# Optimization experiments

Hardware: AMD Instinct MI355X
Metric: run time of the kernel (lower is better)

The kernel has to match this reference:

```python
import jax, jax.numpy as jnp
import numpy as np

D_MODEL, D_K, D_V, H = 1024, 64, 64, 16
B, NQ, NK = 2, 2048, 2048


def setup_inputs() -> dict:
    key = jax.random.key(0)
    ks = jax.random.split(key, 12)
    hd = H * D_K
    xav = lambda k, shape: jax.random.uniform(k, shape, jnp.float32, -1.0, 1.0) * np.sqrt(6.0 / (shape[0] + shape[1]))
    return {
        "queries": jax.random.normal(ks[0], (B, NQ, D_MODEL), jnp.float32),
        "keys": jax.random.normal(ks[1], (B, NK, D_MODEL), jnp.float32),
        "values": jax.random.normal(ks[2], (B, NK, D_MODEL), jnp.float32),
        "memory": jax.random.uniform(ks[3], (B, NK), jnp.float32),
        "Wq": xav(ks[4], (D_MODEL, hd)), "bq": jnp.zeros((hd,), jnp.float32),
        "Wk": xav(ks[5], (D_MODEL, hd)), "bk": jnp.zeros((hd,), jnp.float32),
        "Wv": xav(ks[6], (D_MODEL, H * D_V)), "bv": jnp.zeros((H * D_V,), jnp.float32),
        "Wo": xav(ks[7], (H * D_V, D_MODEL)), "bo": jnp.zeros((D_MODEL,), jnp.float32),
        "Wmm": xav(ks[8], (1, H * D_V)), "bmm": jnp.zeros((H * D_V,), jnp.float32),
    }


def reference(queries, keys, values, memory, Wq, bq, Wk, bk, Wv, bv, Wo, bo, Wmm, bmm):
    b, nq = queries.shape[:2]
    nk = keys.shape[1]
    # projections -> (b, h, n, d)
    q = (queries @ Wq + bq).reshape(b, nq, H, D_K).transpose(0, 2, 1, 3)
    k = (keys @ Wk + bk).reshape(b, nk, H, D_K).transpose(0, 2, 1, 3)
    v = (values @ Wv + bv).reshape(b, nk, H, D_V).transpose(0, 2, 1, 3)
    # memory gate: fc_mm(memory[..., None]) -> (b, nk, h*d_k) -> (b, h, nk, d_k)
    mm = (memory[:, :, None] * Wmm[0] + bmm).reshape(b, nk, H, D_K).transpose(0, 2, 1, 3)
    att = jnp.einsum("bhqd,bhkd->bhqk", q, k * mm) / np.sqrt(D_K).astype(np.float32)
    att = jax.nn.softmax(att, axis=-1)
    out = jnp.einsum("bhqk,bhkd->bhqd", att, v * mm)
    out = out.transpose(0, 2, 1, 3).reshape(b, nq, H * D_V)
    return out @ Wo + bo
```

## Files before the change

### kernel.cpp

```cpp
#include <hip/hip_runtime.h>
#include <hip/hip_bf16.h>

#define H_   16
#define NQ_  2048
#define NK_  2048
#define DM_  1024

typedef float f32x4 __attribute__((ext_vector_type(4)));
typedef float f32x16 __attribute__((ext_vector_type(16)));
typedef __bf16 bf16x8 __attribute__((ext_vector_type(8)));
typedef unsigned short u16x8 __attribute__((ext_vector_type(8)));
typedef unsigned short u16x4 __attribute__((ext_vector_type(4)));

__device__ __forceinline__ unsigned short bfbits(float x) {
  __bf16 h = (__bf16)x;
  return __builtin_bit_cast(unsigned short, h);
}

__global__ __launch_bounds__(256) void prep(
    const float* __restrict__ Wq, const float* __restrict__ Wk,
    const float* __restrict__ Wv, const float* __restrict__ Wo,
    unsigned short* __restrict__ WqT, unsigned short* __restrict__ WkT,
    unsigned short* __restrict__ WvT, unsigned short* __restrict__ WoT,
    const float* __restrict__ q, const float* __restrict__ k, const float* __restrict__ v,
    unsigned short* __restrict__ qo, unsigned short* __restrict__ ko,
    unsigned short* __restrict__ vo) {
  __shared__ float t[64][65];
  const int flat = blockIdx.x;
  if (flat < 1024) {
    const int z = flat >> 8, bx = (flat >> 4) & 15, by = flat & 15;
    const float* src = (z == 0) ? Wq : (z == 1) ? Wk : (z == 2) ? Wv : Wo;
    unsigned short* dst = (z == 0) ? WqT : (z == 1) ? WkT : (z == 2) ? WvT : WoT;
    const int r0 = bx * 64, c0 = by * 64;
    for (int i = threadIdx.x; i < 4096; i += 256) {
      int r = i >> 6, c = i & 63;
      t[r][c] = src[(size_t)(r0 + r) * DM_ + c0 + c];
    }
    __syncthreads();
    for (int i = threadIdx.x; i < 4096; i += 256) {
      int n = i >> 6, kk = i & 63;
      dst[(size_t)(c0 + n) * DM_ + r0 + kk] = bfbits(t[kk][n]);
    }
  } else {
    const int tt = flat - 1024;
    const int which = tt >> 11;
    const float* src = (which == 0) ? q : (which == 1) ? k : v;
    unsigned short* dst = (which == 0) ? qo : (which == 1) ? ko : vo;
    const int i = (tt & 2047) * 256 + threadIdx.x;
    const float4* s4 = (const float4*)src;
    float4 a = s4[2 * i], b = s4[2 * i + 1];
    bf16x8 o;
    o[0] = (__bf16)a.x; o[1] = (__bf16)a.y; o[2] = (__bf16)a.z; o[3] = (__bf16)a.w;
    o[4] = (__bf16)b.x; o[5] = (__bf16)b.y; o[6] = (__bf16)b.z; o[7] = (__bf16)b.w;
    *((bf16x8*)dst + i) = o;
  }
}

__device__ __forceinline__ void gll16(const unsigned short* g, unsigned short* l) {
  __builtin_amdgcn_global_load_lds((const __attribute__((address_space(1))) void*)g,
                                   (__attribute__((address_space(3))) void*)l, 16, 0, 0);
}

template <int MODE>
__device__ __forceinline__ void gemm128_body(
    int bx, int by,
    const unsigned short* __restrict__ A, const unsigned short* __restrict__ Bt, int K,
    const float* __restrict__ bias, const float* __restrict__ mem,
    const float* __restrict__ Wmm, const float* __restrict__ bmm,
    unsigned short* __restrict__ obf,
    unsigned short* Al, unsigned short* Bl) {
  const int tid = threadIdx.x, lane = tid & 63, w = tid >> 6;
  const int wm = w >> 1, wn = w & 1;
  const int m0 = bx * 128, n0 = by * 128;
  const int lrow = lane >> 2, lcol = (lane & 3) * 8;
  const int fr = lane & 15, fk = (lane >> 4) * 8;
  constexpr int TSZ = 128 * 32;

  f32x4 acc[4][4] = {};

  const unsigned short* ag0 = A + (size_t)(m0 + w * 32 + lrow) * K + lcol;
  const unsigned short* bg0 = Bt + (size_t)(n0 + w * 32 + lrow) * K + lcol;
  const int oa0 = (w * 32) * 32, oa1 = (w * 32 + 16) * 32;
  const size_t s16K = (size_t)16 * K;

  const int KT = K >> 5;
  gll16(ag0, Al + oa0); gll16(ag0 + s16K, Al + oa1);
  gll16(bg0, Bl + oa0); gll16(bg0 + s16K, Bl + oa1);
  ag0 += 32; bg0 += 32;
  __syncthreads();

  for (int kt = 0; kt < KT; ++kt) {
    const int cb = (kt & 1) * TSZ;
    const int sb = TSZ - cb;
    if (kt + 1 < KT) {
      gll16(ag0, Al + sb + oa0); gll16(ag0 + s16K, Al + sb + oa1);
      gll16(bg0, Bl + sb + oa0); gll16(bg0 + s16K, Bl + sb + oa1);
      ag0 += 32; bg0 += 32;
    }
    bf16x8 af[4], bfr[4];
#pragma unroll
    for (int i = 0; i < 4; ++i)
      af[i] = *(const bf16x8*)&Al[cb + (wm * 64 + i * 16 + fr) * 32 + fk];
#pragma unroll
    for (int j = 0; j < 4; ++j)
      bfr[j] = *(const bf16x8*)&Bl[cb + (wn * 64 + j * 16 + fr) * 32 + fk];
#pragma unroll
    for (int i = 0; i < 4; ++i)
#pragma unroll
      for (int j = 0; j < 4; ++j)
        acc[i][j] = __builtin_amdgcn_mfma_f32_16x16x32_bf16(af[i], bfr[j], acc[i][j], 0, 0, 0);
    __syncthreads();
  }

#pragma unroll
  for (int i = 0; i < 4; ++i) {
    const int rowb = m0 + wm * 64 + i * 16 + (lane >> 4) * 4;
#pragma unroll
    for (int j = 0; j < 4; ++j) {
      const int col = n0 + wn * 64 + j * 16 + fr;
#pragma unroll
      for (int r = 0; r < 4; ++r) {
        float v = acc[i][j][r];
        int rr = rowb + r;
        if (MODE == 0) {
          int b = rr >> 11, nq = rr & 2047, h = col >> 6, d = col & 63;
          float val = (v + bias[col]) * 0.180336884f;
          obf[(((size_t)(b * H_ + h)) * NQ_ + nq) * 64 + d] = bfbits(val);
        } else if (MODE == 1) {
          int b = rr >> 11, nk = rr & 2047, h = col >> 6, d = col & 63;
          float gate = mem[b * NK_ + nk] * Wmm[col] + bmm[col];
          float val = (v + bias[col]) * gate;
          obf[(((size_t)(b * H_ + h)) * NK_ + nk) * 64 + d] = bfbits(val);
        } else {
          int b = col >> 11, key = col & 2047, h = rr >> 6, d = rr & 63;
          float gate = mem[b * NK_ + key] * Wmm[rr] + bmm[rr];
          float val = (v + bias[rr]) * gate;
          int keyp = (key & ~12) | ((key & 4) << 1) | ((key & 8) >> 1);
          obf[(((size_t)(b * H_ + h)) * 64 + d) * NK_ + keyp] = bfbits(val);
        }
      }
    }
  }
}

__global__ __launch_bounds__(256) void gemm_qkv3(
    const unsigned short* __restrict__ qbf, const unsigned short* __restrict__ kbf,
    const unsigned short* __restrict__ vbf, const unsigned short* __restrict__ WvT,
    const unsigned short* __restrict__ WqT, const unsigned short* __restrict__ WkT,
    const float* __restrict__ bq, const float* __restrict__ bk, const float* __restrict__ bv,
    const float* __restrict__ mem, const float* __restrict__ Wmm, const float* __restrict__ bmm,
    unsigned short* __restrict__ Qp, unsigned short* __restrict__ Kp,
    unsigned short* __restrict__ VpT) {
  __shared__ unsigned short Al[2 * 128 * 32];
  __shared__ unsigned short Bl[2 * 128 * 32];
  const int gid = (blockIdx.x & 7) * 96 + (blockIdx.x >> 3);
  if (gid < 256) {
    gemm128_body<0>(gid & 31, gid >> 5, qbf, WqT, 1024, bq, nullptr, nullptr, nullptr,
                    Qp, Al, Bl);
  } else if (gid < 512) {
    int bb = gid - 256;
    gemm128_body<1>(bb & 31, bb >> 5, kbf, WkT, 1024, bk, mem, Wmm, bmm, Kp, Al, Bl);
  } else {
    int bb = gid - 512;
    gemm128_body<2>(bb & 7, bb >> 3, WvT, vbf, 1024, bv, mem, Wmm, bmm, VpT, Al, Bl);
  }
}

__global__ __launch_bounds__(256) void gemm_out(
    const unsigned short* __restrict__ AO, const unsigned short* __restrict__ WoT,
    const float* __restrict__ bo, float* __restrict__ out) {
  __shared__ unsigned short Al[2 * 64 * 32];
  __shared__ unsigned short Bl[2 * 128 * 32];
  const int b = (blockIdx.x & 7) * 64 + (blockIdx.x >> 3);
  const int bx = b & 63, by = b >> 6;
  const int tid = threadIdx.x, lane = tid & 63, w = tid >> 6;
  const int wm = w >> 1, wn = w & 1;
  const int m0 = bx * 64, n0 = by * 128;
  const int lrow = lane >> 2, lcol = (lane & 3) * 8;
  const int fr = lane & 15, fk = (lane >> 4) * 8;
  const int K = 1024;
  constexpr int TA = 64 * 32, TB = 128 * 32;

  f32x4 acc[2][4] = {};

  const unsigned short* ag = AO + (size_t)(m0 + w * 16 + lrow) * K + lcol;
  const unsigned short* bg = WoT + (size_t)(n0 + w * 32 + lrow) * K + lcol;
  const int oa = (w * 16) * 32;
  const int ob0 = (w * 32) * 32, ob1 = (w * 32 + 16) * 32;
  const size_t s16K = (size_t)16 * K;

  gll16(ag, Al + oa);
  gll16(bg, Bl + ob0); gll16(bg + s16K, Bl + ob1);
  ag += 32; bg += 32;
  __syncthreads();

  for (int kt = 0; kt < 32; ++kt) {
    const int ca = (kt & 1) * TA, cbb = (kt & 1) * TB;
    const int sa = TA - ca, sbb = TB - cbb;
    if (kt + 1 < 32) {
      gll16(ag, Al + sa + oa);
      gll16(bg, Bl + sbb + ob0); gll16(bg + s16K, Bl + sbb + ob1);
      ag += 32; bg += 32;
    }
    bf16x8 af[2], bfr[4];
#pragma unroll
    for (int i = 0; i < 2; ++i)
      af[i] = *(const bf16x8*)&Al[ca + (wm * 32 + i * 16 + fr) * 32 + fk];
#pragma unroll
    for (int j = 0; j < 4; ++j)
      bfr[j] = *(const bf16x8*)&Bl[cbb + (wn * 64 + j * 16 + fr) * 32 + fk];
#pragma unroll
    for (int i = 0; i < 2; ++i)
#pragma unroll
      for (int j = 0; j < 4; ++j)
        acc[i][j] = __builtin_amdgcn_mfma_f32_16x16x32_bf16(af[i], bfr[j], acc[i][j], 0, 0, 0);
    __syncthreads();
  }

#pragma unroll
  for (int i = 0; i < 2; ++i) {
    const int rowb = m0 + wm * 32 + i * 16 + (lane >> 4) * 4;
#pragma unroll
    for (int j = 0; j < 4; ++j) {
      const int col = n0 + wn * 64 + j * 16 + fr;
#pragma unroll
      for (int r = 0; r < 4; ++r)
        out[(size_t)(rowb + r) * DM_ + col] = acc[i][j][r] + bo[col];
    }
  }
}

__global__ __launch_bounds__(256, 2) void flash_attn(const unsigned short* __restrict__ Qp,
                                                     const unsigned short* __restrict__ Kp,
                                                     const unsigned short* __restrict__ VpT,
                                                     unsigned short* __restrict__ AO) {
  __shared__ unsigned short Ks[2][128][66];
  __shared__ unsigned short Vs[2][64][130];

  const int tid = threadIdx.x, lane = tid & 63, w = tid >> 6;
  const int gid = (blockIdx.x & 7) * 64 + (blockIdx.x >> 3);
  const int bh = gid >> 4;
  const int qt = gid & 15;
  const int r31 = lane & 31, hi2 = lane >> 5;

  const unsigned short* qg = Qp + (((size_t)bh * NQ_) + qt * 128 + w * 32 + r31) * 64 + hi2 * 8;
  bf16x8 qf[4];
#pragma unroll
  for (int s = 0; s < 4; ++s) qf[s] = *(const bf16x8*)&qg[s * 16];

  const int krow = tid >> 1, kcol = (tid & 1) * 32;
  const int vrow = tid >> 2, vcol = (tid & 3) * 32;
  const unsigned short* kg = Kp + ((size_t)bh * NK_ + krow) * 64 + kcol;
  const unsigned short* vg = VpT + ((size_t)bh * 64 + vrow) * NK_ + vcol;

  f32x16 acc0 = {}, acc1 = {};
  float l_run = 0.0f;

  u16x8 kr[4], vr[4];
#pragma unroll
  for (int i = 0; i < 4; ++i) {
    kr[i] = *(const u16x8*)(kg + 8 * i);
    vr[i] = *(const u16x8*)(vg + 8 * i);
  }
#pragma unroll
  for (int i = 0; i < 4; ++i) {
    *(u16x8*)&Ks[0][krow][kcol + 8 * i] = kr[i];
    *(u16x8*)&Vs[0][vrow][vcol + 8 * i] = vr[i];
  }

  for (int kt = 0; kt < 16; ++kt) {
    const int cur = kt & 1;
    __syncthreads();

    f32x16 sv[4] = {};
    __builtin_amdgcn_s_setprio(1);
#pragma unroll
    for (int s = 0; s < 4; ++s) {
#pragma unroll
      for (int kb = 0; kb < 4; ++kb) {
        bf16x8 ka = *(const bf16x8*)&Ks[cur][kb * 32 + r31][s * 16 + hi2 * 8];
        sv[kb] = __builtin_amdgcn_mfma_f32_32x32x16_bf16(ka, qf[s], sv[kb], 0, 0, 0);
      }
    }
    __builtin_amdgcn_s_setprio(0);

    if (kt + 1 < 16) {
      const unsigned short* kn = kg + (size_t)(kt + 1) * 128 * 64;
      const unsigned short* vn = vg + (kt + 1) * 128;
#pragma unroll
      for (int i = 0; i < 4; ++i) {
        kr[i] = *(const u16x8*)(kn + 8 * i);
        vr[i] = *(const u16x8*)(vn + 8 * i);
      }
    }

    float psp[4] = {0.f, 0.f, 0.f, 0.f};
    bf16x8 pb[8];
#pragma unroll
    for (int kb = 0; kb < 4; ++kb) {
#pragma unroll
      for (int g = 0; g < 16; ++g) {
        float p = __builtin_amdgcn_exp2f(sv[kb][g]);
        psp[kb] += p;
        pb[2 * kb + (g >> 3)][g & 7] = (__bf16)p;
      }
    }
    float ps = (psp[0] + psp[1]) + (psp[2] + psp[3]);
    ps += __shfl_xor(ps, 32);
    l_run += ps;

    __builtin_amdgcn_s_setprio(1);
#pragma unroll
    for (int ks = 0; ks < 8; ++ks) {
      bf16x8 va0 = *(const bf16x8*)&Vs[cur][r31][ks * 16 + hi2 * 8];
      bf16x8 va1 = *(const bf16x8*)&Vs[cur][32 + r31][ks * 16 + hi2 * 8];
      acc0 = __builtin_amdgcn_mfma_f32_32x32x16_bf16(va0, pb[ks], acc0, 0, 0, 0);
      acc1 = __builtin_amdgcn_mfma_f32_32x32x16_bf16(va1, pb[ks], acc1, 0, 0, 0);
    }
    __builtin_amdgcn_s_setprio(0);

    if (kt + 1 < 16) {
#pragma unroll
      for (int i = 0; i < 4; ++i) {
        *(u16x8*)&Ks[cur ^ 1][krow][kcol + 8 * i] = kr[i];
        *(u16x8*)&Vs[cur ^ 1][vrow][vcol + 8 * i] = vr[i];
      }
    }
  }

  const int b = bh >> 4, h = bh & 15;
  const float linv = 1.0f / l_run;
  const int qrow = qt * 128 + w * 32 + r31;
  const size_t rowbase = (((size_t)b * NQ_ + qrow) << 10) + h * 64;
#pragma unroll
  for (int c = 0; c < 4; ++c) {
    u16x4 o0, o1;
#pragma unroll
    for (int i = 0; i < 4; ++i) {
      o0[i] = bfbits(acc0[c * 4 + i] * linv);
      o1[i] = bfbits(acc1[c * 4 + i] * linv);
    }
    *(u16x4*)&AO[rowbase + 8 * c + 4 * hi2]      = o0;
    *(u16x4*)&AO[rowbase + 32 + 8 * c + 4 * hi2] = o1;
  }
}

extern "C" void kernel_launch(void* const* d_in, const int* in_sizes, int n_in,
                              void* d_out, int out_size, void* d_ws, size_t ws_size,
                              hipStream_t stream) {
  const float* queries = (const float*)d_in[0];
  const float* keys    = (const float*)d_in[1];
  const float* values  = (const float*)d_in[2];
  const float* memory  = (const float*)d_in[3];
  const float* Wq  = (const float*)d_in[4];
  const float* bq  = (const float*)d_in[5];
  const float* Wk  = (const float*)d_in[6];
  const float* bk  = (const float*)d_in[7];
  const float* Wv  = (const float*)d_in[8];
  const float* bv  = (const float*)d_in[9];
  const float* Wo  = (const float*)d_in[10];
  const float* bo  = (const float*)d_in[11];
  const float* Wmm = (const float*)d_in[12];
  const float* bmm = (const float*)d_in[13];

  char* ws = (char*)d_ws;
  const size_t SZ_X = (size_t)4096 * 1024 * 2;
  const size_t SZ_W = (size_t)1024 * 1024 * 2;
  unsigned short* qbf = (unsigned short*)(ws);
  unsigned short* kbf = (unsigned short*)(ws + SZ_X);
  unsigned short* vbf = (unsigned short*)(ws + 2 * SZ_X);
  unsigned short* AO  = (unsigned short*)(ws);
  size_t off = 3 * SZ_X;
  unsigned short* WqT = (unsigned short*)(ws + off); off += SZ_W;
  unsigned short* WkT = (unsigned short*)(ws + off); off += SZ_W;
  unsigned short* WvT = (unsigned short*)(ws + off); off += SZ_W;
  unsigned short* WoT = (unsigned short*)(ws + off); off += SZ_W;
  unsigned short* Qp  = (unsigned short*)(ws + off); off += SZ_X;
  unsigned short* Kp  = (unsigned short*)(ws + off); off += SZ_X;
  unsigned short* VpT = (unsigned short*)(ws + off); off += SZ_X;

  prep<<<7168, 256, 0, stream>>>(Wq, Wk, Wv, Wo, WqT, WkT, WvT, WoT,
                                 queries, keys, values, qbf, kbf, vbf);

  gemm_qkv3<<<768, 256, 0, stream>>>(qbf, kbf, vbf, WvT, WqT, WkT,
                                     bq, bk, bv, memory, Wmm, bmm, Qp, Kp, VpT);

  flash_attn<<<512, 256, 0, stream>>>(Qp, Kp, VpT, AO);

  gemm_out<<<512, 256, 0, stream>>>(AO, WoT, bo, (float*)d_out);
}
```

Measured before the change: 124.7 us.

## Double per-wave query rows in flash attention to reuse K/V tiles

Each wave now processes 64 query rows (two 32-row fragments) instead of 32, so every K and V fragment read from LDS feeds two MFMAs, and each block covers 256 query rows. The grid shrinks from 512 to 256 blocks and launch bounds drop to one block per SM to make room for the doubled accumulator and score registers. The intent is to halve K/V global and LDS traffic per query row, at the cost of lower occupancy and a grid of 256 blocks that may leave some of the GPU's 256 CUs with little latency hiding.

```diff
diff --git a/kernel.cpp b/kernel.cpp
--- a/kernel.cpp
+++ b/kernel.cpp
@@ -230,7 +230,7 @@
   }
 }
 
-__global__ __launch_bounds__(256, 2) void flash_attn(const unsigned short* __restrict__ Qp,
+__global__ __launch_bounds__(256, 1) void flash_attn(const unsigned short* __restrict__ Qp,
                                                      const unsigned short* __restrict__ Kp,
                                                      const unsigned short* __restrict__ VpT,
                                                      unsigned short* __restrict__ AO) {
@@ -238,23 +238,26 @@
   __shared__ unsigned short Vs[2][64][130];
 
   const int tid = threadIdx.x, lane = tid & 63, w = tid >> 6;
-  const int gid = (blockIdx.x & 7) * 64 + (blockIdx.x >> 3);
-  const int bh = gid >> 4;
-  const int qt = gid & 15;
+  const int gid = (blockIdx.x & 7) * 32 + (blockIdx.x >> 3);
+  const int bh = gid >> 3;
+  const int qt = gid & 7;
   const int r31 = lane & 31, hi2 = lane >> 5;
 
-  const unsigned short* qg = Qp + (((size_t)bh * NQ_) + qt * 128 + w * 32 + r31) * 64 + hi2 * 8;
-  bf16x8 qf[4];
-#pragma unroll
-  for (int s = 0; s < 4; ++s) qf[s] = *(const bf16x8*)&qg[s * 16];
+  const unsigned short* qg = Qp + (((size_t)bh * NQ_) + qt * 256 + w * 64 + r31) * 64 + hi2 * 8;
+  bf16x8 qf0[4], qf1[4];
+#pragma unroll
+  for (int s = 0; s < 4; ++s) {
+    qf0[s] = *(const bf16x8*)&qg[s * 16];
+    qf1[s] = *(const bf16x8*)&qg[32 * 64 + s * 16];
+  }
 
   const int krow = tid >> 1, kcol = (tid & 1) * 32;
   const int vrow = tid >> 2, vcol = (tid & 3) * 32;
   const unsigned short* kg = Kp + ((size_t)bh * NK_ + krow) * 64 + kcol;
   const unsigned short* vg = VpT + ((size_t)bh * 64 + vrow) * NK_ + vcol;
 
-  f32x16 acc0 = {}, acc1 = {};
-  float l_run = 0.0f;
+  f32x16 acc00 = {}, acc10 = {}, acc01 = {}, acc11 = {};
+  float l0 = 0.0f, l1 = 0.0f;
 
   u16x8 kr[4], vr[4];
 #pragma unroll
@@ -272,14 +275,15 @@
     const int cur = kt & 1;
     __syncthreads();
 
-    f32x16 sv[4] = {};
+    f32x16 sv0[4] = {}, sv1[4] = {};
     __builtin_amdgcn_s_setprio(1);
 #pragma unroll
     for (int s = 0; s < 4; ++s) {
 #pragma unroll
       for (int kb = 0; kb < 4; ++kb) {
         bf16x8 ka = *(const bf16x8*)&Ks[cur][kb * 32 + r31][s * 16 + hi2 * 8];
-        sv[kb] = __builtin_amdgcn_mfma_f32_32x32x16_bf16(ka, qf[s], sv[kb], 0, 0, 0);
+        sv0[kb] = __builtin_amdgcn_mfma_f32_32x32x16_bf16(ka, qf0[s], sv0[kb], 0, 0, 0);
+        sv1[kb] = __builtin_amdgcn_mfma_f32_32x32x16_bf16(ka, qf1[s], sv1[kb], 0, 0, 0);
       }
     }
     __builtin_amdgcn_s_setprio(0);
@@ -294,28 +298,31 @@
       }
     }
 
-    float psp[4] = {0.f, 0.f, 0.f, 0.f};
-    bf16x8 pb[8];
+    float ps0 = 0.f, ps1 = 0.f;
+    bf16x8 pb0[8], pb1[8];
 #pragma unroll
     for (int kb = 0; kb < 4; ++kb) {
 #pragma unroll
       for (int g = 0; g < 16; ++g) {
-        float p = __builtin_amdgcn_exp2f(sv[kb][g]);
-        psp[kb] += p;
-        pb[2 * kb + (g >> 3)][g & 7] = (__bf16)p;
+        float pA = __builtin_amdgcn_exp2f(sv0[kb][g]);
+        float pB = __builtin_amdgcn_exp2f(sv1[kb][g]);
+        ps0 += pA; ps1 += pB;
+        pb0[2 * kb + (g >> 3)][g & 7] = (__bf16)pA;
+        pb1[2 * kb + (g >> 3)][g & 7] = (__bf16)pB;
       }
     }
-    float ps = (psp[0] + psp[1]) + (psp[2] + psp[3]);
-    ps += __shfl_xor(ps, 32);
-    l_run += ps;
+    ps0 += __shfl_xor(ps0, 32); l0 += ps0;
+    ps1 += __shfl_xor(ps1, 32); l1 += ps1;
 
     __builtin_amdgcn_s_setprio(1);
 #pragma unroll
     for (int ks = 0; ks < 8; ++ks) {
       bf16x8 va0 = *(const bf16x8*)&Vs[cur][r31][ks * 16 + hi2 * 8];
       bf16x8 va1 = *(const bf16x8*)&Vs[cur][32 + r31][ks * 16 + hi2 * 8];
-      acc0 = __builtin_amdgcn_mfma_f32_32x32x16_bf16(va0, pb[ks], acc0, 0, 0, 0);
-      acc1 = __builtin_amdgcn_mfma_f32_32x32x16_bf16(va1, pb[ks], acc1, 0, 0, 0);
+      acc00 = __builtin_amdgcn_mfma_f32_32x32x16_bf16(va0, pb0[ks], acc00, 0, 0, 0);
+      acc10 = __builtin_amdgcn_mfma_f32_32x32x16_bf16(va1, pb0[ks], acc10, 0, 0, 0);
+      acc01 = __builtin_amdgcn_mfma_f32_32x32x16_bf16(va0, pb1[ks], acc01, 0, 0, 0);
+      acc11 = __builtin_amdgcn_mfma_f32_32x32x16_bf16(va1, pb1[ks], acc11, 0, 0, 0);
     }
     __builtin_amdgcn_s_setprio(0);
 
@@ -329,19 +336,24 @@
   }
 
   const int b = bh >> 4, h = bh & 15;
-  const float linv = 1.0f / l_run;
-  const int qrow = qt * 128 + w * 32 + r31;
-  const size_t rowbase = (((size_t)b * NQ_ + qrow) << 10) + h * 64;
+  const float linv0 = 1.0f / l0, linv1 = 1.0f / l1;
+  const int qrow0 = qt * 256 + w * 64 + r31;
+  const size_t rowbase0 = (((size_t)b * NQ_ + qrow0) << 10) + h * 64;
+  const size_t rowbase1 = (((size_t)b * NQ_ + qrow0 + 32) << 10) + h * 64;
 #pragma unroll
   for (int c = 0; c < 4; ++c) {
-    u16x4 o0, o1;
+    u16x4 o00, o10, o01, o11;
 #pragma unroll
     for (int i = 0; i < 4; ++i) {
-      o0[i] = bfbits(acc0[c * 4 + i] * linv);
-      o1[i] = bfbits(acc1[c * 4 + i] * linv);
-    }
-    *(u16x4*)&AO[rowbase + 8 * c + 4 * hi2]      = o0;
-    *(u16x4*)&AO[rowbase + 32 + 8 * c + 4 * hi2] = o1;
+      o00[i] = bfbits(acc00[c * 4 + i] * linv0);
+      o10[i] = bfbits(acc10[c * 4 + i] * linv0);
+      o01[i] = bfbits(acc01[c * 4 + i] * linv1);
+      o11[i] = bfbits(acc11[c * 4 + i] * linv1);
+    }
+    *(u16x4*)&AO[rowbase0 + 8 * c + 4 * hi2]      = o00;
+    *(u16x4*)&AO[rowbase0 + 32 + 8 * c + 4 * hi2] = o10;
+    *(u16x4*)&AO[rowbase1 + 8 * c + 4 * hi2]      = o01;
+    *(u16x4*)&AO[rowbase1 + 32 + 8 * c + 4 * hi2] = o11;
   }
 }
 
@@ -385,7 +397,7 @@
   gemm_qkv3<<<768, 256, 0, stream>>>(qbf, kbf, vbf, WvT, WqT, WkT,
                                      bq, bk, bv, memory, Wmm, bmm, Qp, Kp, VpT);
 
-  flash_attn<<<512, 256, 0, stream>>>(Qp, Kp, VpT, AO);
+  flash_attn<<<256, 256, 0, stream>>>(Qp, Kp, VpT, AO);
 
   gemm_out<<<512, 256, 0, stream>>>(AO, WoT, bo, (float*)d_out);
 }
```

New measurement: 130.2 us. +4.4%, slower.

## Fuse fp32-to-bf16 activation conversion into QKV projection GEMM loads

Applied to the files above, without the earlier changes.

Drops the prep kernel's separate pass that turned queries/keys/values into bf16. The QKV GEMM now reads fp32 activations straight into registers one stage ahead, converts them to bf16 and writes them to LDS, which removes a full write and re-read of three 8MB bf16 buffers. The tile index mapping for the Q/K GEMMs is also swapped (row-major block order). Register-staged loads replace async global_load_lds for those operands, so there is more register pressure and less overlap, and each fp32 activation tile is read by the 8 column-tile blocks that use it.

```diff
diff --git a/kernel.cpp b/kernel.cpp
--- a/kernel.cpp
+++ b/kernel.cpp
@@ -17,42 +17,30 @@
   return __builtin_bit_cast(unsigned short, h);
 }
 
+__device__ __forceinline__ bf16x8 cvt8(float4 a, float4 b) {
+  bf16x8 o;
+  o[0] = (__bf16)a.x; o[1] = (__bf16)a.y; o[2] = (__bf16)a.z; o[3] = (__bf16)a.w;
+  o[4] = (__bf16)b.x; o[5] = (__bf16)b.y; o[6] = (__bf16)b.z; o[7] = (__bf16)b.w;
+  return o;
+}
+
 __global__ __launch_bounds__(256) void prep(
-    const float* __restrict__ Wq, const float* __restrict__ Wk,
-    const float* __restrict__ Wv, const float* __restrict__ Wo,
-    unsigned short* __restrict__ WqT, unsigned short* __restrict__ WkT,
-    unsigned short* __restrict__ WvT, unsigned short* __restrict__ WoT,
-    const float* __restrict__ q, const float* __restrict__ k, const float* __restrict__ v,
-    unsigned short* __restrict__ qo, unsigned short* __restrict__ ko,
-    unsigned short* __restrict__ vo) {
+    const float* __restrict__ s0, const float* __restrict__ s1,
+    const float* __restrict__ s2, const float* __restrict__ s3,
+    unsigned short* __restrict__ d0, unsigned short* __restrict__ d1,
+    unsigned short* __restrict__ d2, unsigned short* __restrict__ d3) {
+  const float* src = (blockIdx.z == 0) ? s0 : (blockIdx.z == 1) ? s1 : (blockIdx.z == 2) ? s2 : s3;
+  unsigned short* dst = (blockIdx.z == 0) ? d0 : (blockIdx.z == 1) ? d1 : (blockIdx.z == 2) ? d2 : d3;
   __shared__ float t[64][65];
-  const int flat = blockIdx.x;
-  if (flat < 1024) {
-    const int z = flat >> 8, bx = (flat >> 4) & 15, by = flat & 15;
-    const float* src = (z == 0) ? Wq : (z == 1) ? Wk : (z == 2) ? Wv : Wo;
-    unsigned short* dst = (z == 0) ? WqT : (z == 1) ? WkT : (z == 2) ? WvT : WoT;
-    const int r0 = bx * 64, c0 = by * 64;
-    for (int i = threadIdx.x; i < 4096; i += 256) {
-      int r = i >> 6, c = i & 63;
-      t[r][c] = src[(size_t)(r0 + r) * DM_ + c0 + c];
-    }
-    __syncthreads();
-    for (int i = threadIdx.x; i < 4096; i += 256) {
-      int n = i >> 6, kk = i & 63;
-      dst[(size_t)(c0 + n) * DM_ + r0 + kk] = bfbits(t[kk][n]);
-    }
-  } else {
-    const int tt = flat - 1024;
-    const int which = tt >> 11;
-    const float* src = (which == 0) ? q : (which == 1) ? k : v;
-    unsigned short* dst = (which == 0) ? qo : (which == 1) ? ko : vo;
-    const int i = (tt & 2047) * 256 + threadIdx.x;
-    const float4* s4 = (const float4*)src;
-    float4 a = s4[2 * i], b = s4[2 * i + 1];
-    bf16x8 o;
-    o[0] = (__bf16)a.x; o[1] = (__bf16)a.y; o[2] = (__bf16)a.z; o[3] = (__bf16)a.w;
-    o[4] = (__bf16)b.x; o[5] = (__bf16)b.y; o[6] = (__bf16)b.z; o[7] = (__bf16)b.w;
-    *((bf16x8*)dst + i) = o;
+  const int r0 = blockIdx.x * 64, c0 = blockIdx.y * 64;
+  for (int i = threadIdx.x; i < 4096; i += 256) {
+    int r = i >> 6, c = i & 63;
+    t[r][c] = src[(size_t)(r0 + r) * DM_ + c0 + c];
+  }
+  __syncthreads();
+  for (int i = threadIdx.x; i < 4096; i += 256) {
+    int n = i >> 6, kk = i & 63;
+    dst[(size_t)(c0 + n) * DM_ + r0 + kk] = bfbits(t[kk][n]);
   }
 }
 
@@ -64,11 +52,13 @@
 template <int MODE>
 __device__ __forceinline__ void gemm128_body(
     int bx, int by,
-    const unsigned short* __restrict__ A, const unsigned short* __restrict__ Bt, int K,
+    const void* __restrict__ Av, const void* __restrict__ Btv, int K,
     const float* __restrict__ bias, const float* __restrict__ mem,
     const float* __restrict__ Wmm, const float* __restrict__ bmm,
     unsigned short* __restrict__ obf,
     unsigned short* Al, unsigned short* Bl) {
+  constexpr bool AF32 = (MODE <= 1);
+  constexpr bool BF32 = (MODE == 2);
   const int tid = threadIdx.x, lane = tid & 63, w = tid >> 6;
   const int wm = w >> 1, wn = w & 1;
   const int m0 = bx * 128, n0 = by * 128;
@@ -78,24 +68,79 @@
 
   f32x4 acc[4][4] = {};
 
-  const unsigned short* ag0 = A + (size_t)(m0 + w * 32 + lrow) * K + lcol;
-  const unsigned short* bg0 = Bt + (size_t)(n0 + w * 32 + lrow) * K + lcol;
+  const size_t aoff = (size_t)(m0 + w * 32 + lrow) * K + lcol;
+  const size_t boff = (size_t)(n0 + w * 32 + lrow) * K + lcol;
+  const unsigned short* agb = (const unsigned short*)Av + aoff;
+  const float*          agf = (const float*)Av + aoff;
+  const unsigned short* bgb = (const unsigned short*)Btv + boff;
+  const float*          bgf = (const float*)Btv + boff;
+  const int os0 = (w * 32 + lrow) * 32 + lcol;
+  const int os1 = (w * 32 + lrow + 16) * 32 + lcol;
   const int oa0 = (w * 32) * 32, oa1 = (w * 32 + 16) * 32;
   const size_t s16K = (size_t)16 * K;
 
+  float4 fa0, fa1, fa2, fa3;
+  float4 fb0, fb1, fb2, fb3;
+
   const int KT = K >> 5;
-  gll16(ag0, Al + oa0); gll16(ag0 + s16K, Al + oa1);
-  gll16(bg0, Bl + oa0); gll16(bg0 + s16K, Bl + oa1);
-  ag0 += 32; bg0 += 32;
+  if constexpr (AF32) {
+    fa0 = *(const float4*)agf; fa1 = *(const float4*)(agf + 4);
+    fa2 = *(const float4*)(agf + s16K); fa3 = *(const float4*)(agf + s16K + 4);
+    *(bf16x8*)(Al + os0) = cvt8(fa0, fa1);
+    *(bf16x8*)(Al + os1) = cvt8(fa2, fa3);
+    agf += 32;
+    fa0 = *(const float4*)agf; fa1 = *(const float4*)(agf + 4);
+    fa2 = *(const float4*)(agf + s16K); fa3 = *(const float4*)(agf + s16K + 4);
+    agf += 32;
+  } else {
+    gll16(agb, Al + oa0); gll16(agb + s16K, Al + oa1);
+    agb += 32;
+  }
+  if constexpr (BF32) {
+    fb0 = *(const float4*)bgf; fb1 = *(const float4*)(bgf + 4);
+    fb2 = *(const float4*)(bgf + s16K); fb3 = *(const float4*)(bgf + s16K + 4);
+    *(bf16x8*)(Bl + os0) = cvt8(fb0, fb1);
+    *(bf16x8*)(Bl + os1) = cvt8(fb2, fb3);
+    bgf += 32;
+    fb0 = *(const float4*)bgf; fb1 = *(const float4*)(bgf + 4);
+    fb2 = *(const float4*)(bgf + s16K); fb3 = *(const float4*)(bgf + s16K + 4);
+    bgf += 32;
+  } else {
+    gll16(bgb, Bl + oa0); gll16(bgb + s16K, Bl + oa1);
+    bgb += 32;
+  }
   __syncthreads();
 
   for (int kt = 0; kt < KT; ++kt) {
     const int cb = (kt & 1) * TSZ;
     const int sb = TSZ - cb;
     if (kt + 1 < KT) {
-      gll16(ag0, Al + sb + oa0); gll16(ag0 + s16K, Al + sb + oa1);
-      gll16(bg0, Bl + sb + oa0); gll16(bg0 + s16K, Bl + sb + oa1);
-      ag0 += 32; bg0 += 32;
+      if constexpr (AF32) {
+        *(bf16x8*)(Al + sb + os0) = cvt8(fa0, fa1);
+        *(bf16x8*)(Al + sb + os1) = cvt8(fa2, fa3);
+      } else {
+        gll16(agb, Al + sb + oa0); gll16(agb + s16K, Al + sb + oa1);
+        agb += 32;
+      }
+      if constexpr (BF32) {
+        *(bf16x8*)(Bl + sb + os0) = cvt8(fb0, fb1);
+        *(bf16x8*)(Bl + sb + os1) = cvt8(fb2, fb3);
+      } else {
+        gll16(bgb, Bl + sb + oa0); gll16(bgb + s16K, Bl + sb + oa1);
+        bgb += 32;
+      }
+    }
+    if (kt + 2 < KT) {
+      if constexpr (AF32) {
+        fa0 = *(const float4*)agf; fa1 = *(const float4*)(agf + 4);
+        fa2 = *(const float4*)(agf + s16K); fa3 = *(const float4*)(agf + s16K + 4);
+        agf += 32;
+      }
+      if constexpr (BF32) {
+        fb0 = *(const float4*)bgf; fb1 = *(const float4*)(bgf + 4);
+        fb2 = *(const float4*)(bgf + s16K); fb3 = *(const float4*)(bgf + s16K + 4);
+        bgf += 32;
+      }
     }
     bf16x8 af[4], bfr[4];
 #pragma unroll
@@ -144,8 +189,8 @@
 }
 
 __global__ __launch_bounds__(256) void gemm_qkv3(
-    const unsigned short* __restrict__ qbf, const unsigned short* __restrict__ kbf,
-    const unsigned short* __restrict__ vbf, const unsigned short* __restrict__ WvT,
+    const float* __restrict__ queries, const float* __restrict__ keys,
+    const float* __restrict__ values, const unsigned short* __restrict__ WvT,
     const unsigned short* __restrict__ WqT, const unsigned short* __restrict__ WkT,
     const float* __restrict__ bq, const float* __restrict__ bk, const float* __restrict__ bv,
     const float* __restrict__ mem, const float* __restrict__ Wmm, const float* __restrict__ bmm,
@@ -155,14 +200,14 @@
   __shared__ unsigned short Bl[2 * 128 * 32];
   const int gid = (blockIdx.x & 7) * 96 + (blockIdx.x >> 3);
   if (gid < 256) {
-    gemm128_body<0>(gid & 31, gid >> 5, qbf, WqT, 1024, bq, nullptr, nullptr, nullptr,
+    gemm128_body<0>(gid >> 3, gid & 7, queries, WqT, 1024, bq, nullptr, nullptr, nullptr,
                     Qp, Al, Bl);
   } else if (gid < 512) {
     int bb = gid - 256;
-    gemm128_body<1>(bb & 31, bb >> 5, kbf, WkT, 1024, bk, mem, Wmm, bmm, Kp, Al, Bl);
+    gemm128_body<1>(bb >> 3, bb & 7, keys, WkT, 1024, bk, mem, Wmm, bmm, Kp, Al, Bl);
   } else {
     int bb = gid - 512;
-    gemm128_body<2>(bb & 7, bb >> 3, WvT, vbf, 1024, bv, mem, Wmm, bmm, VpT, Al, Bl);
+    gemm128_body<2>(bb & 7, bb >> 3, WvT, values, 1024, bv, mem, Wmm, bmm, VpT, Al, Bl);
   }
 }
 
@@ -364,25 +409,19 @@
   const float* bmm = (const float*)d_in[13];
 
   char* ws = (char*)d_ws;
-  const size_t SZ_X = (size_t)4096 * 1024 * 2;
-  const size_t SZ_W = (size_t)1024 * 1024 * 2;
-  unsigned short* qbf = (unsigned short*)(ws);
-  unsigned short* kbf = (unsigned short*)(ws + SZ_X);
-  unsigned short* vbf = (unsigned short*)(ws + 2 * SZ_X);
+  const size_t MB = 1024 * 1024;
   unsigned short* AO  = (unsigned short*)(ws);
-  size_t off = 3 * SZ_X;
-  unsigned short* WqT = (unsigned short*)(ws + off); off += SZ_W;
-  unsigned short* WkT = (unsigned short*)(ws + off); off += SZ_W;
-  unsigned short* WvT = (unsigned short*)(ws + off); off += SZ_W;
-  unsigned short* WoT = (unsigned short*)(ws + off); off += SZ_W;
-  unsigned short* Qp  = (unsigned short*)(ws + off); off += SZ_X;
-  unsigned short* Kp  = (unsigned short*)(ws + off); off += SZ_X;
-  unsigned short* VpT = (unsigned short*)(ws + off); off += SZ_X;
-
-  prep<<<7168, 256, 0, stream>>>(Wq, Wk, Wv, Wo, WqT, WkT, WvT, WoT,
-                                 queries, keys, values, qbf, kbf, vbf);
-
-  gemm_qkv3<<<768, 256, 0, stream>>>(qbf, kbf, vbf, WvT, WqT, WkT,
+  unsigned short* WqT = (unsigned short*)(ws + 8 * MB);
+  unsigned short* WkT = (unsigned short*)(ws + 10 * MB);
+  unsigned short* WvT = (unsigned short*)(ws + 12 * MB);
+  unsigned short* WoT = (unsigned short*)(ws + 14 * MB);
+  unsigned short* Qp  = (unsigned short*)(ws + 16 * MB);
+  unsigned short* Kp  = (unsigned short*)(ws + 24 * MB);
+  unsigned short* VpT = (unsigned short*)(ws + 32 * MB);
+
+  prep<<<dim3(16, 16, 4), 256, 0, stream>>>(Wq, Wk, Wv, Wo, WqT, WkT, WvT, WoT);
+
+  gemm_qkv3<<<768, 256, 0, stream>>>(queries, keys, values, WvT, WqT, WkT,
                                      bq, bk, bv, memory, Wmm, bmm, Qp, Kp, VpT);
 
   flash_attn<<<512, 256, 0, stream>>>(Qp, Kp, VpT, AO);
```

Result: faster. 119.5 us (-4.2%).
